# Kernel optimization log

Hardware: AMD Instinct MI355X
Metric: run time of the kernel (lower is better)

The kernel has to match this reference:

```python
import jax, jax.numpy as jnp
import numpy as np
from jax import lax

B, T = 2, 2
BT = B * T
C = 256
NH, DH = 8, 32
NL, NP = 3, 4
NLAYERS = 6
DFF = 1024
SHAPES = [(16, 16), (32, 32), (64, 64)]  # coarse -> fine, last is finest
STARTS = [0, 256, 1280]
LQ = 5376
H4 = W4 = 128
EPS = 1e-5


def setup_inputs():
    key = jax.random.key(0)
    ks = iter(jax.random.split(key, 64))
    def nrm(shape, s=0.02):
        return jax.random.normal(next(ks), shape, jnp.float32) * s
    inp = {}
    for l, (H, W) in enumerate(SHAPES):
        inp[f"src{l}"] = jax.random.normal(next(ks), (BT, C, H, W), jnp.float32)
        inp[f"pos{l}"] = jax.random.normal(next(ks), (BT, C, H, W), jnp.float32)
    inp["mask_features"] = jax.random.normal(next(ks), (B, C, T, H4, W4), jnp.float32)
    inp["level_embed"] = nrm((NL, C), 1.0)
    inp["off_w"] = nrm((NLAYERS, C, NH * NL * NP * 2), 0.01)
    inp["off_b"] = nrm((NLAYERS, NH * NL * NP * 2), 0.1)
    inp["aw_w"] = nrm((NLAYERS, C, NH * NL * NP))
    inp["aw_b"] = jnp.zeros((NLAYERS, NH * NL * NP), jnp.float32)
    inp["val_w"] = nrm((NLAYERS, C, C), 0.05)
    inp["val_b"] = jnp.zeros((NLAYERS, C), jnp.float32)
    inp["out_w"] = nrm((NLAYERS, C, C), 0.05)
    inp["out_b"] = jnp.zeros((NLAYERS, C), jnp.float32)
    inp["ln1_g"] = jnp.ones((NLAYERS, C), jnp.float32)
    inp["ln1_b"] = jnp.zeros((NLAYERS, C), jnp.float32)
    inp["ff1_w"] = nrm((NLAYERS, C, DFF))
    inp["ff1_b"] = jnp.zeros((NLAYERS, DFF), jnp.float32)
    inp["ff2_w"] = nrm((NLAYERS, DFF, C))
    inp["ff2_b"] = jnp.zeros((NLAYERS, C), jnp.float32)
    inp["ln2_g"] = jnp.ones((NLAYERS, C), jnp.float32)
    inp["ln2_b"] = jnp.zeros((NLAYERS, C), jnp.float32)
    inp["lat_w"] = nrm((NLAYERS, C, C, 1, 1), 0.05)
    inp["lat_b"] = jnp.zeros((NLAYERS, C), jnp.float32)
    inp["outc_w"] = nrm((NLAYERS, C, C, 3, 3), 0.02)
    inp["outc_b"] = jnp.zeros((NLAYERS, C), jnp.float32)
    return inp


def _ln(x, g, b):
    m = x.mean(-1, keepdims=True)
    v = ((x - m) ** 2).mean(-1, keepdims=True)
    return (x - m) * lax.rsqrt(v + EPS) * g + b


def _conv(x, w, b, pad):
    y = lax.conv_general_dilated(x, w, (1, 1), [(pad, pad), (pad, pad)],
                                 dimension_numbers=("NCHW", "OIHW", "NCHW"))
    return y + b[None, :, None, None]


def _sample_level(v_l, loc, H, W):
    # v_l: (BT, NH, H*W, DH); loc: (BT, LQ, NH, NP, 2) normalized [0,1]
    # grid_sample bilinear, align_corners=False, zero padding:
    # pixel coord = loc * size - 0.5
    bt, nh, _, dh = v_l.shape
    x = loc[..., 0] * W - 0.5
    y = loc[..., 1] * H - 0.5
    x0 = jnp.floor(x)
    y0 = jnp.floor(y)
    x0i = x0.astype(jnp.int32)
    y0i = y0.astype(jnp.int32)
    fx = (x - x0).transpose(0, 2, 1, 3)[..., None]  # (BT,NH,LQ,NP,1)
    fy = (y - y0).transpose(0, 2, 1, 3)[..., None]
    def gather(ix, iy):
        valid = (ix >= 0) & (ix < W) & (iy >= 0) & (iy < H)
        idx = jnp.clip(iy, 0, H - 1) * W + jnp.clip(ix, 0, W - 1)
        idx = idx.transpose(0, 2, 1, 3)  # (BT,NH,LQ,NP)
        Lq, P = idx.shape[2], idx.shape[3]
        g = jnp.take_along_axis(v_l, idx.reshape(bt, nh, Lq * P)[..., None], axis=2)
        g = g.reshape(bt, nh, Lq, P, dh)
        return g * valid.transpose(0, 2, 1, 3)[..., None]
    v00 = gather(x0i, y0i)
    v01 = gather(x0i + 1, y0i)
    v10 = gather(x0i, y0i + 1)
    v11 = gather(x0i + 1, y0i + 1)
    return (v00 * (1 - fx) * (1 - fy) + v01 * fx * (1 - fy)
            + v10 * (1 - fx) * fy + v11 * fx * fy)


def _ref_points():
    pts = []
    for (H, W) in SHAPES:
        ys = (jnp.arange(H, dtype=jnp.float32) + 0.5) / H
        xs = (jnp.arange(W, dtype=jnp.float32) + 0.5) / W
        gy, gx = jnp.meshgrid(ys, xs, indexing="ij")
        pts.append(jnp.stack([gx.reshape(-1), gy.reshape(-1)], -1))
    return jnp.concatenate(pts, 0)  # (LQ, 2); valid_ratios are all ones


def reference(src0, src1, src2, pos0, pos1, pos2, mask_features, level_embed,
              off_w, off_b, aw_w, aw_b, val_w, val_b, out_w, out_b,
              ln1_g, ln1_b, ff1_w, ff1_b, ff2_w, ff2_b, ln2_g, ln2_b,
              lat_w, lat_b, outc_w, outc_b):
    srcs = [src0, src1, src2]
    poss = [pos0, pos1, pos2]
    output = jnp.concatenate([s.reshape(BT, C, -1).transpose(0, 2, 1) for s in srcs], 1)
    posf = jnp.concatenate(
        [p.reshape(BT, C, -1).transpose(0, 2, 1) + level_embed[l][None, None]
         for l, p in enumerate(poss)], 1)
    refp = _ref_points()
    norm = jnp.array([[W, H] for (H, W) in SHAPES], jnp.float32)  # (NL,2) as (W,H)
    lh, lw = SHAPES[-1]
    for i in range(NLAYERS):
        q = output + posf
        v = (output @ val_w[i] + val_b[i]).reshape(BT, LQ, NH, DH)
        off = (q @ off_w[i] + off_b[i]).reshape(BT, LQ, NH, NL, NP, 2)
        aw = jax.nn.softmax((q @ aw_w[i] + aw_b[i]).reshape(BT, LQ, NH, NL * NP), -1)
        aw = aw.reshape(BT, LQ, NH, NL, NP)
        loc = refp[None, :, None, None, None, :] + off / norm[None, None, None, :, None, :]
        acc = jnp.zeros((BT, NH, LQ, DH), output.dtype)
        for l, (H, W) in enumerate(SHAPES):
            v_l = v[:, STARTS[l]:STARTS[l] + H * W].transpose(0, 2, 1, 3)
            s = _sample_level(v_l, loc[:, :, :, l], H, W)
            acc = acc + (s * aw[:, :, :, l].transpose(0, 2, 1, 3)[..., None]).sum(3)
        attn = acc.transpose(0, 2, 1, 3).reshape(BT, LQ, C) @ out_w[i] + out_b[i]
        output = _ln(output + attn, ln1_g[i], ln1_b[i])
        ff = jax.nn.relu(output @ ff1_w[i] + ff1_b[i]) @ ff2_w[i] + ff2_b[i]
        output = _ln(output + ff, ln2_g[i], ln2_b[i])
        # FPN fusion with the finest transformer level
        lm = output[:, STARTS[-1]:].reshape(BT, lh, lw, C).transpose(0, 3, 1, 2)
        x = mask_features.transpose(0, 2, 1, 3, 4).reshape(B * T, C, H4, W4)
        x = _conv(x, lat_w[i], lat_b[i], 0)
        x = x + jax.image.resize(lm, (BT, C, H4, W4), method="bilinear")
        x = jax.nn.relu(_conv(x, outc_w[i], outc_b[i], 1))
        mask_features = mask_features + x.reshape(B, T, C, H4, W4).transpose(0, 2, 1, 3, 4)
    return output, mask_features
```

## Files before the change

### kernel.cpp

```cpp
#include <hip/hip_runtime.h>

#define DEV __device__ __forceinline__

using f32x4  = __attribute__((ext_vector_type(4))) float;
using bf16x8 = __attribute__((ext_vector_type(8))) short;

static constexpr int kLQ = 5376;

DEV unsigned short f2b(float f) {
  unsigned u = __builtin_bit_cast(unsigned, f);
  u = u + 0x7fffu + ((u >> 16) & 1u);
  return (unsigned short)(u >> 16);
}
DEV float b2f(unsigned short s) {
  unsigned u = ((unsigned)s) << 16;
  return __builtin_bit_cast(float, u);
}

DEV void glds16(const void* g, void* l) {
  __builtin_amdgcn_global_load_lds(
      (const __attribute__((address_space(1))) void*)g,
      (__attribute__((address_space(3))) void*)l, 16, 0, 0);
}

template<int EPI>
__global__ __launch_bounds__(256) void gemm128(
    const unsigned short* __restrict__ A, const unsigned short* __restrict__ Bt,
    const float* __restrict__ bias, void* __restrict__ Cp,
    int M, int N, int K, const float* __restrict__ rsrc)
{
  __shared__ unsigned short As[128 * 32];
  __shared__ unsigned short Bs[128 * 32];
  const int tid = threadIdx.x, lane = tid & 63, wid = tid >> 6;
  const int m0 = blockIdx.x * 128, n0 = blockIdx.y * 128;
  const int wr = wid >> 1, wc = wid & 1;
  const int l15 = lane & 15, lg = lane >> 4;

  const int s0 = wid * 64 + lane, s1 = 256 + s0;
  const int r0 = s0 >> 2, cs0 = (s0 & 3) ^ ((r0 >> 1) & 3);
  const int r1 = s1 >> 2, cs1 = (s1 & 3) ^ ((r1 >> 1) & 3);
  const unsigned short* Ag0 = A + (long)(m0 + r0) * K + cs0 * 8;
  const unsigned short* Ag1 = A + (long)(m0 + r1) * K + cs1 * 8;
  const unsigned short* Bg0 = Bt + (long)(n0 + r0) * K + cs0 * 8;
  const unsigned short* Bg1 = Bt + (long)(n0 + r1) * K + cs1 * 8;
  unsigned short* Al0 = As + (wid * 64) * 8;
  unsigned short* Al1 = As + (256 + wid * 64) * 8;
  unsigned short* Bl0 = Bs + (wid * 64) * 8;
  unsigned short* Bl1 = Bs + (256 + wid * 64) * 8;

  f32x4 acc[4][4];
#pragma unroll
  for (int i = 0; i < 4; i++)
#pragma unroll
    for (int j = 0; j < 4; j++) acc[i][j] = f32x4{0.f, 0.f, 0.f, 0.f};

  for (int k0 = 0; k0 < K; k0 += 32) {
    glds16(Ag0 + k0, Al0);
    glds16(Ag1 + k0, Al1);
    glds16(Bg0 + k0, Bl0);
    glds16(Bg1 + k0, Bl1);
    __syncthreads();
    bf16x8 a[4], b[4];
#pragma unroll
    for (int i = 0; i < 4; i++) {
      int ra = wr * 64 + i * 16 + l15;
      a[i] = *(const bf16x8*)(As + ra * 32 + (lg ^ ((ra >> 1) & 3)) * 8);
      int rb = wc * 64 + i * 16 + l15;
      b[i] = *(const bf16x8*)(Bs + rb * 32 + (lg ^ ((rb >> 1) & 3)) * 8);
    }
#pragma unroll
    for (int mi = 0; mi < 4; mi++)
#pragma unroll
      for (int nj = 0; nj < 4; nj++)
        acc[mi][nj] = __builtin_amdgcn_mfma_f32_16x16x32_bf16(
            a[mi], b[nj], acc[mi][nj], 0, 0, 0);
    __syncthreads();
  }

  int ry0 = 0, ry1 = 0;
  float rfy = 0.f;
  const float* rb0 = nullptr;
  if (EPI == 3) {
    const int bt = m0 >> 14, y = (m0 & 16383) >> 7;
    float sy = y * 0.5f - 0.25f;
    float y0f = floorf(sy);
    rfy = sy - y0f;
    ry0 = min(63, max(0, (int)y0f));
    ry1 = min(63, max(0, (int)y0f + 1));
    rb0 = rsrc + ((long)bt * kLQ + 1280) * 256;
  }

#pragma unroll
  for (int mi = 0; mi < 4; mi++)
#pragma unroll
    for (int nj = 0; nj < 4; nj++) {
      int col = n0 + wc * 64 + nj * 16 + l15;
      if (col >= N) continue;
      float bb = bias[col];
#pragma unroll
      for (int rr = 0; rr < 4; rr++) {
        long row = m0 + wr * 64 + mi * 16 + lg * 4 + rr;
        float v = acc[mi][nj][rr] + bb;
        if (EPI == 2) v = fmaxf(v, 0.f);
        if (EPI == 3) {
          int x = wr * 64 + mi * 16 + lg * 4 + rr;
          float sx = x * 0.5f - 0.25f;
          float x0f = floorf(sx);
          float fx = sx - x0f;
          int x0 = min(63, max(0, (int)x0f)), x1 = min(63, max(0, (int)x0f + 1));
          float v00 = rb0[(long)(ry0 * 64 + x0) * 256 + col];
          float v01 = rb0[(long)(ry0 * 64 + x1) * 256 + col];
          float v10 = rb0[(long)(ry1 * 64 + x0) * 256 + col];
          float v11 = rb0[(long)(ry1 * 64 + x1) * 256 + col];
          v += (1.f - rfy) * ((1.f - fx) * v00 + fx * v01)
             + rfy * ((1.f - fx) * v10 + fx * v11);
        }
        if (EPI == 0) ((float*)Cp)[row * N + col] = v;
        else ((unsigned short*)Cp)[row * N + col] = f2b(v);
      }
    }
}

__global__ __launch_bounds__(256) void conv3x3(
    const unsigned short* __restrict__ xb, const unsigned short* __restrict__ wT,
    const float* __restrict__ bias, float* __restrict__ mf,
    unsigned short* __restrict__ mc)
{
  __shared__ unsigned short As[3 * 128 * 32];
  const int tid = threadIdx.x, lane = tid & 63, wid = tid >> 6;
  const int y = blockIdx.x, c0 = blockIdx.y * 128, bt = blockIdx.z;
  const int wr = wid >> 1, wc = wid & 1;
  const int l15 = lane & 15, lg = lane >> 4;
  const unsigned short* xbb = xb + (long)bt * (16384 * 256);
  const bool zr0 = (y == 0), zr2 = (y == 127);

  f32x4 acc[4][4];
#pragma unroll
  for (int i = 0; i < 4; i++)
#pragma unroll
    for (int j = 0; j < 4; j++) acc[i][j] = f32x4{0.f, 0.f, 0.f, 0.f};

  for (int s = 0; s < 8; s++) {
    const int ci0 = s * 32;
#pragma unroll
    for (int k = 0; k < 6; k++) {
      const int S = k * 256 + tid;
      const int r = S >> 9;
      const int p = (S >> 2) & 127;
      const int cs = (S & 3) ^ ((p >> 1) & 3);
      if ((r == 0 && zr0) || (r == 2 && zr2)) {
        *(uint4*)(As + S * 8) = uint4{0u, 0u, 0u, 0u};
      } else {
        glds16(xbb + ((long)((y + r - 1) * 128 + p) * 256 + ci0 + cs * 8),
               As + (k * 256 + wid * 64) * 8);
      }
    }
    __syncthreads();
#pragma unroll
    for (int r = 0; r < 3; r++) {
#pragma unroll
      for (int dxi = 0; dxi < 3; dxi++) {
        const int t = r * 3 + dxi, dx = dxi - 1;
        const unsigned short* wb = wT + (((long)t * 8 + s) * 256) * 32;
        bf16x8 a[4], b[4];
#pragma unroll
        for (int i = 0; i < 4; i++) {
          const int co_r = c0 + wc * 64 + i * 16 + l15;
          b[i] = *(const bf16x8*)(wb + co_r * 32 + lg * 8);
          const int px = wr * 64 + i * 16 + l15 + dx;
          const int pxc = min(127, max(0, px));
          bf16x8 v = *(const bf16x8*)(
              As + ((r * 128 + pxc) * 4 + (lg ^ ((pxc >> 1) & 3))) * 8);
          if ((unsigned)px >= 128u) v = bf16x8{0, 0, 0, 0, 0, 0, 0, 0};
          a[i] = v;
        }
#pragma unroll
        for (int mi = 0; mi < 4; mi++)
#pragma unroll
          for (int nj = 0; nj < 4; nj++)
            acc[mi][nj] = __builtin_amdgcn_mfma_f32_16x16x32_bf16(
                a[mi], b[nj], acc[mi][nj], 0, 0, 0);
      }
    }
    __syncthreads();
  }

#pragma unroll
  for (int mi = 0; mi < 4; mi++)
#pragma unroll
    for (int nj = 0; nj < 4; nj++) {
      int co = c0 + wc * 64 + nj * 16 + l15;
      float bb = bias[co];
#pragma unroll
      for (int rr = 0; rr < 4; rr++) {
        int x = wr * 64 + mi * 16 + lg * 4 + rr;
        long idx = ((long)bt * 16384 + y * 128 + x) * 256 + co;
        float v = mf[idx] + fmaxf(acc[mi][nj][rr] + bb, 0.f);
        mf[idx] = v;
        mc[idx] = f2b(v);
      }
    }
}

__global__ __launch_bounds__(256) void deform_sample(
    const float* __restrict__ offp, const float* __restrict__ awlog,
    const unsigned short* __restrict__ vp, unsigned short* __restrict__ attn)
{
  const int m = blockIdx.x * 4 + (threadIdx.x >> 6);
  const int t = threadIdx.x & 63;
  const int h = t >> 3, d4 = t & 7;
  const int bt = m / kLQ, q = m % kLQ;
  int pq, Wq;
  if (q < 256)       { pq = q;        Wq = 16; }
  else if (q < 1280) { pq = q - 256;  Wq = 32; }
  else               { pq = q - 1280; Wq = 64; }
  const float refx = ((pq % Wq) + 0.5f) / Wq;
  const float refy = ((pq / Wq) + 0.5f) / Wq;
  const int starts[3] = {0, 256, 1280};
  const int dims[3]   = {16, 32, 64};

  const float4* offr = (const float4*)(offp + (long)m * 192 + h * 24);
  const float4* awr  = (const float4*)(awlog + (long)m * 96 + h * 12);
  float off[24], aw[12];
#pragma unroll
  for (int j = 0; j < 6; j++) {
    float4 v = offr[j];
    off[j * 4] = v.x; off[j * 4 + 1] = v.y; off[j * 4 + 2] = v.z; off[j * 4 + 3] = v.w;
  }
#pragma unroll
  for (int j = 0; j < 3; j++) {
    float4 v = awr[j];
    aw[j * 4] = v.x; aw[j * 4 + 1] = v.y; aw[j * 4 + 2] = v.z; aw[j * 4 + 3] = v.w;
  }
  float mx = aw[0];
#pragma unroll
  for (int j = 1; j < 12; j++) mx = fmaxf(mx, aw[j]);
  float ssum = 0.f;
#pragma unroll
  for (int j = 0; j < 12; j++) { float e = __expf(aw[j] - mx); aw[j] = e; ssum += e; }
  float inv = 1.f / ssum;

  const unsigned short* vb = vp + ((long)bt * kLQ) * 256 + h * 32 + d4 * 4;
  float ax = 0.f, ay = 0.f, az = 0.f, aww = 0.f;
#pragma unroll
  for (int l = 0; l < 3; l++) {
    const int Wl = dims[l];
    const float winv = 1.f / (float)Wl;
    const int st = starts[l];
#pragma unroll
    for (int p = 0; p < 4; p++) {
      float ox = off[l * 8 + p * 2], oy = off[l * 8 + p * 2 + 1];
      float a  = aw[l * 4 + p] * inv;
      float fxp = (refx + ox * winv) * Wl - 0.5f;
      float fyp = (refy + oy * winv) * Wl - 0.5f;
      float x0f = floorf(fxp), y0f = floorf(fyp);
      int x0 = (int)x0f, y0 = (int)y0f;
      float fx = fxp - x0f, fy = fyp - y0f;
      float sx = 0.f, sy = 0.f, sz = 0.f, sw = 0.f;
#pragma unroll
      for (int cy = 0; cy < 2; cy++)
#pragma unroll
        for (int cx = 0; cx < 2; cx++) {
          int ix = x0 + cx, iy = y0 + cy;
          if ((unsigned)ix < (unsigned)Wl && (unsigned)iy < (unsigned)Wl) {
            float w = (cx ? fx : 1.f - fx) * (cy ? fy : 1.f - fy);
            ushort4 u = *(const ushort4*)(vb + (long)(st + iy * Wl + ix) * 256);
            sx += w * b2f(u.x); sy += w * b2f(u.y);
            sz += w * b2f(u.z); sw += w * b2f(u.w);
          }
        }
      ax += a * sx; ay += a * sy; az += a * sz; aww += a * sw;
    }
  }
  ushort4 r;
  r.x = f2b(ax); r.y = f2b(ay); r.z = f2b(az); r.w = f2b(aww);
  *(ushort4*)(attn + (long)m * 256 + h * 32 + d4 * 4) = r;
}

template<bool QB>
__global__ __launch_bounds__(256) void ln_row(
    float* __restrict__ out, const float* __restrict__ delta,
    const float* __restrict__ g, const float* __restrict__ b,
    unsigned short* __restrict__ ob, const float* __restrict__ posf,
    unsigned short* __restrict__ qb)
{
  const long m = blockIdx.x * 4 + (threadIdx.x >> 6);
  const int lane = threadIdx.x & 63;
  const long base = m * 256 + lane * 4;
  float4 a = *(const float4*)(out + base);
  float4 d = *(const float4*)(delta + base);
  float x0 = a.x + d.x, x1 = a.y + d.y, x2 = a.z + d.z, x3 = a.w + d.w;
  float s = x0 + x1 + x2 + x3;
#pragma unroll
  for (int o = 32; o > 0; o >>= 1) s += __shfl_xor(s, o);
  float mean = s * (1.f / 256.f);
  float d0 = x0 - mean, d1 = x1 - mean, d2 = x2 - mean, d3 = x3 - mean;
  float s2 = d0 * d0 + d1 * d1 + d2 * d2 + d3 * d3;
#pragma unroll
  for (int o = 32; o > 0; o >>= 1) s2 += __shfl_xor(s2, o);
  float rs = rsqrtf(s2 * (1.f / 256.f) + 1e-5f);
  float4 gv = *(const float4*)(g + lane * 4);
  float4 bv = *(const float4*)(b + lane * 4);
  float r0 = d0 * rs * gv.x + bv.x, r1 = d1 * rs * gv.y + bv.y;
  float r2 = d2 * rs * gv.z + bv.z, r3 = d3 * rs * gv.w + bv.w;
  *(float4*)(out + base) = float4{r0, r1, r2, r3};
  ushort4 o4; o4.x = f2b(r0); o4.y = f2b(r1); o4.z = f2b(r2); o4.w = f2b(r3);
  *(ushort4*)(ob + base) = o4;
  if (QB) {
    float4 pf = *(const float4*)(posf + base);
    ushort4 q4;
    q4.x = f2b(r0 + pf.x); q4.y = f2b(r1 + pf.y);
    q4.z = f2b(r2 + pf.z); q4.w = f2b(r3 + pf.w);
    *(ushort4*)(qb + base) = q4;
  }
}

__global__ __launch_bounds__(256) void wtrans_pad(
    const float* __restrict__ in, unsigned short* __restrict__ outT,
    int K, int N, int Npad)
{
  int idx = blockIdx.x * 256 + threadIdx.x;
  if (idx >= Npad * K) return;
  int n = idx / K, k = idx % K;
  unsigned short v = 0;
  if (n < N) v = f2b(in[(long)blockIdx.z * K * N + (long)k * N + n]);
  outT[(long)blockIdx.z * Npad * K + idx] = v;
}

__global__ __launch_bounds__(256) void wconvert(
    const float* __restrict__ in, unsigned short* __restrict__ out, int n)
{
  int idx = blockIdx.x * 256 + threadIdx.x;
  if (idx < n) out[idx] = f2b(in[idx]);
}

__global__ __launch_bounds__(256) void wpermconv(
    const float* __restrict__ in, unsigned short* __restrict__ out)
{
  int idx = blockIdx.x * 256 + threadIdx.x;
  const int ci = idx & 255;
  const int co = (idx >> 8) & 255;
  const int t  = (idx >> 16) % 9;
  const int l  = idx / (9 << 16);
  const int s = ci >> 5, cin = ci & 31;
  out[((((long)l * 9 + t) * 8 + s) * 256 + co) * 32 + cin] =
      f2b(in[(((long)l * 256 + co) * 256 + ci) * 9 + t]);
}

__global__ __launch_bounds__(256) void init_level(
    const float* __restrict__ src, const float* __restrict__ pos,
    const float* __restrict__ emb, float* __restrict__ outp,
    float* __restrict__ posf, unsigned short* __restrict__ ob,
    unsigned short* __restrict__ qb, int HW, int start)
{
  __shared__ float t1[32][33];
  __shared__ float t2[32][33];
  const int bt = blockIdx.z;
  const int p0 = blockIdx.x * 32, c0 = blockIdx.y * 32;
  const int tx = threadIdx.x, ty = threadIdx.y;
  const float* sb = src + ((long)bt * 256 + c0) * HW + p0;
  const float* pb = pos + ((long)bt * 256 + c0) * HW + p0;
#pragma unroll
  for (int j = 0; j < 4; j++) {
    int cc = ty + j * 8;
    t1[cc][tx] = sb[(long)cc * HW + tx];
    t2[cc][tx] = pb[(long)cc * HW + tx];
  }
  __syncthreads();
#pragma unroll
  for (int j = 0; j < 4; j++) {
    int pp = ty + j * 8;
    long row = (long)bt * kLQ + start + p0 + pp;
    float v = t1[tx][pp];
    float pv = t2[tx][pp] + emb[c0 + tx];
    outp[row * 256 + c0 + tx] = v;
    ob[row * 256 + c0 + tx] = f2b(v);
    qb[row * 256 + c0 + tx] = f2b(v + pv);
    posf[row * 256 + c0 + tx] = pv;
  }
}

__global__ __launch_bounds__(256) void init_mask(
    const float* __restrict__ in, float* __restrict__ mf,
    unsigned short* __restrict__ mc)
{
  __shared__ float t[32][33];
  const int bt = blockIdx.z, b = bt >> 1, tt = bt & 1;
  const int p0 = blockIdx.x * 32, c0 = blockIdx.y * 32;
  const int tx = threadIdx.x, ty = threadIdx.y;
  const float* base = in + (((long)b * 256 + c0) * 2 + tt) * 16384 + p0;
#pragma unroll
  for (int j = 0; j < 4; j++) {
    int cc = ty + j * 8;
    t[cc][tx] = base[(long)cc * 32768 + tx];
  }
  __syncthreads();
#pragma unroll
  for (int j = 0; j < 4; j++) {
    int pp = ty + j * 8;
    long idx = ((long)bt * 16384 + p0 + pp) * 256 + c0 + tx;
    float v = t[tx][pp];
    mf[idx] = v;
    mc[idx] = f2b(v);
  }
}

__global__ __launch_bounds__(256) void hwc_to_out(
    const float* __restrict__ mf, float* __restrict__ outm)
{
  __shared__ float t[32][33];
  const int bt = blockIdx.z, b = bt >> 1, tt = bt & 1;
  const int p0 = blockIdx.x * 32, c0 = blockIdx.y * 32;
  const int tx = threadIdx.x, ty = threadIdx.y;
#pragma unroll
  for (int j = 0; j < 4; j++) {
    int pp = ty + j * 8;
    t[pp][tx] = mf[((long)bt * 16384 + p0 + pp) * 256 + c0 + tx];
  }
  __syncthreads();
#pragma unroll
  for (int j = 0; j < 4; j++) {
    int cc = ty + j * 8;
    outm[(((long)b * 256 + c0 + cc) * 2 + tt) * 16384 + p0 + tx] = t[tx][cc];
  }
}

extern "C" void kernel_launch(void* const* d_in, const int* in_sizes, int n_in,
                              void* d_out, int out_size, void* d_ws, size_t ws_size,
                              hipStream_t stream)
{
  const float* src[3] = {(const float*)d_in[0], (const float*)d_in[2], (const float*)d_in[4]};
  const float* pos[3] = {(const float*)d_in[1], (const float*)d_in[3], (const float*)d_in[5]};
  const float* mask_in = (const float*)d_in[6];
  const float* lemb    = (const float*)d_in[7];
  const float* off_w   = (const float*)d_in[8];
  const float* off_b   = (const float*)d_in[9];
  const float* aw_w    = (const float*)d_in[10];
  const float* aw_b    = (const float*)d_in[11];
  const float* val_w   = (const float*)d_in[12];
  const float* val_b   = (const float*)d_in[13];
  const float* out_w   = (const float*)d_in[14];
  const float* out_b   = (const float*)d_in[15];
  const float* ln1_g   = (const float*)d_in[16];
  const float* ln1_b   = (const float*)d_in[17];
  const float* ff1_w   = (const float*)d_in[18];
  const float* ff1_b   = (const float*)d_in[19];
  const float* ff2_w   = (const float*)d_in[20];
  const float* ff2_b   = (const float*)d_in[21];
  const float* ln2_g   = (const float*)d_in[22];
  const float* ln2_b   = (const float*)d_in[23];
  const float* lat_w   = (const float*)d_in[24];
  const float* lat_b   = (const float*)d_in[25];
  const float* outc_w  = (const float*)d_in[26];
  const float* outc_b  = (const float*)d_in[27];

  float* outbuf = (float*)d_out;
  float* maskf  = (float*)d_out + 5505024;

  char* wp = (char*)d_ws;
  auto alloc = [&](size_t bytes) {
    char* p = wp;
    wp += (bytes + 255) & ~(size_t)255;
    return p;
  };
  float*          posf  = (float*)alloc(5505024ull * 4);
  unsigned short* qb    = (unsigned short*)alloc(5505024ull * 2);
  unsigned short* ob    = (unsigned short*)alloc(5505024ull * 2);
  unsigned short* vbuf  = (unsigned short*)alloc(5505024ull * 2);
  float*          offb  = (float*)alloc(4128768ull * 4);
  float*          awb   = (float*)alloc(2064384ull * 4);
  unsigned short* attnb = (unsigned short*)alloc(5505024ull * 2);
  float*          tmp1  = (float*)alloc(5505024ull * 4);
  unsigned short* ffh   = (unsigned short*)alloc(22020096ull * 2);
  unsigned short* mc    = (unsigned short*)alloc(16777216ull * 2);
  unsigned short* xb    = (unsigned short*)alloc(16777216ull * 2);
  float*          mfh   = (float*)alloc(16777216ull * 4);
  unsigned short* valT  = (unsigned short*)alloc(6ull * 65536 * 2);
  unsigned short* offT  = (unsigned short*)alloc(6ull * 65536 * 2);
  unsigned short* awT   = (unsigned short*)alloc(6ull * 32768 * 2);
  unsigned short* outT  = (unsigned short*)alloc(6ull * 65536 * 2);
  unsigned short* ff1T  = (unsigned short*)alloc(6ull * 262144 * 2);
  unsigned short* ff2T  = (unsigned short*)alloc(6ull * 262144 * 2);
  unsigned short* latT  = (unsigned short*)alloc(6ull * 65536 * 2);
  unsigned short* outcT = (unsigned short*)alloc(6ull * 589824 * 2);

  wtrans_pad<<<dim3(256, 1, 6), 256, 0, stream>>>(val_w, valT, 256, 256, 256);
  wtrans_pad<<<dim3(256, 1, 6), 256, 0, stream>>>(off_w, offT, 256, 192, 256);
  wtrans_pad<<<dim3(128, 1, 6), 256, 0, stream>>>(aw_w,  awT,  256, 96, 128);
  wtrans_pad<<<dim3(256, 1, 6), 256, 0, stream>>>(out_w, outT, 256, 256, 256);
  wtrans_pad<<<dim3(1024, 1, 6), 256, 0, stream>>>(ff1_w, ff1T, 256, 1024, 1024);
  wtrans_pad<<<dim3(1024, 1, 6), 256, 0, stream>>>(ff2_w, ff2T, 1024, 256, 256);
  wconvert<<<dim3(1536), 256, 0, stream>>>(lat_w, latT, 6 * 65536);
  wpermconv<<<dim3(13824), 256, 0, stream>>>(outc_w, outcT);

  const int hw[3] = {256, 1024, 4096};
  const int st[3] = {0, 256, 1280};
  for (int l = 0; l < 3; l++)
    init_level<<<dim3(hw[l] / 32, 8, 4), dim3(32, 8), 0, stream>>>(
        src[l], pos[l], lemb + l * 256, outbuf, posf, ob, qb, hw[l], st[l]);
  init_mask<<<dim3(512, 8, 4), dim3(32, 8), 0, stream>>>(mask_in, mfh, mc);

  for (int i = 0; i < 6; i++) {
    gemm128<1><<<dim3(168, 2), 256, 0, stream>>>(
        ob, valT + (long)i * 65536, val_b + i * 256, vbuf, 21504, 256, 256, nullptr);
    gemm128<0><<<dim3(168, 2), 256, 0, stream>>>(
        qb, offT + (long)i * 65536, off_b + i * 192, offb, 21504, 192, 256, nullptr);
    gemm128<0><<<dim3(168, 1), 256, 0, stream>>>(
        qb, awT + (long)i * 32768, aw_b + i * 96, awb, 21504, 96, 256, nullptr);
    deform_sample<<<dim3(5376), 256, 0, stream>>>(offb, awb, vbuf, attnb);
    gemm128<0><<<dim3(168, 2), 256, 0, stream>>>(
        attnb, outT + (long)i * 65536, out_b + i * 256, tmp1, 21504, 256, 256, nullptr);
    ln_row<false><<<dim3(5376), 256, 0, stream>>>(
        outbuf, tmp1, ln1_g + i * 256, ln1_b + i * 256, ob, nullptr, nullptr);
    gemm128<2><<<dim3(168, 8), 256, 0, stream>>>(
        ob, ff1T + (long)i * 262144, ff1_b + i * 1024, ffh, 21504, 1024, 256, nullptr);
    gemm128<0><<<dim3(168, 2), 256, 0, stream>>>(
        ffh, ff2T + (long)i * 262144, ff2_b + i * 256, tmp1, 21504, 256, 1024, nullptr);
    ln_row<true><<<dim3(5376), 256, 0, stream>>>(
        outbuf, tmp1, ln2_g + i * 256, ln2_b + i * 256, ob, posf, qb);
    gemm128<3><<<dim3(512, 2), 256, 0, stream>>>(
        mc, latT + (long)i * 65536, lat_b + i * 256, xb, 65536, 256, 256, outbuf);
    conv3x3<<<dim3(128, 2, 4), 256, 0, stream>>>(
        xb, outcT + (long)i * 589824, outc_b + i * 256, mfh, mc);
  }
  hwc_to_out<<<dim3(512, 8, 4), dim3(32, 8), 0, stream>>>(mfh, maskf);
}
```

Baseline: 2.828 ms.

## Drop fp32 mask accumulator and double-buffer conv3x3 LDS staging

The separate fp32 mask_features buffer is removed; the residual is now kept only in the bf16 copy that conv3x3 reads, updates and writes back, and init_mask and hwc_to_out are changed to match. This cuts the fp32 read and write of the full mask tensor on every layer, at the cost of accumulating the residual in bf16 across six layers, which loses precision. Separately, conv3x3 now uses two LDS buffers so the load of the next input-channel slice is issued while MFMAs run on the current one. This doubles the LDS footprint, which may lower occupancy.

```diff
diff --git a/kernel.cpp b/kernel.cpp
--- a/kernel.cpp
+++ b/kernel.cpp
@@ -123,10 +123,9 @@
 
 __global__ __launch_bounds__(256) void conv3x3(
     const unsigned short* __restrict__ xb, const unsigned short* __restrict__ wT,
-    const float* __restrict__ bias, float* __restrict__ mf,
-    unsigned short* __restrict__ mc)
-{
-  __shared__ unsigned short As[3 * 128 * 32];
+    const float* __restrict__ bias, unsigned short* __restrict__ mc)
+{
+  __shared__ unsigned short As[2 * 3 * 128 * 32];
   const int tid = threadIdx.x, lane = tid & 63, wid = tid >> 6;
   const int y = blockIdx.x, c0 = blockIdx.y * 128, bt = blockIdx.z;
   const int wr = wid >> 1, wc = wid & 1;
@@ -140,22 +139,31 @@
 #pragma unroll
     for (int j = 0; j < 4; j++) acc[i][j] = f32x4{0.f, 0.f, 0.f, 0.f};
 
-  for (int s = 0; s < 8; s++) {
+  auto STAGE = [&](int buf, int s) {
     const int ci0 = s * 32;
+    unsigned short* Ab = As + buf * (3 * 128 * 32);
 #pragma unroll
     for (int k = 0; k < 6; k++) {
       const int S = k * 256 + tid;
-      const int r = S >> 9;
+      const int r = k >> 1;
       const int p = (S >> 2) & 127;
       const int cs = (S & 3) ^ ((p >> 1) & 3);
       if ((r == 0 && zr0) || (r == 2 && zr2)) {
-        *(uint4*)(As + S * 8) = uint4{0u, 0u, 0u, 0u};
+        *(uint4*)(Ab + S * 8) = uint4{0u, 0u, 0u, 0u};
       } else {
         glds16(xbb + ((long)((y + r - 1) * 128 + p) * 256 + ci0 + cs * 8),
-               As + (k * 256 + wid * 64) * 8);
+               Ab + (k * 256 + wid * 64) * 8);
       }
     }
-    __syncthreads();
+  };
+
+  STAGE(0, 0);
+  __syncthreads();
+
+  for (int s = 0; s < 8; s++) {
+    const int cur = s & 1;
+    if (s < 7) STAGE(cur ^ 1, s + 1);
+    const unsigned short* Ab = As + cur * (3 * 128 * 32);
 #pragma unroll
     for (int r = 0; r < 3; r++) {
 #pragma unroll
@@ -170,7 +178,7 @@
           const int px = wr * 64 + i * 16 + l15 + dx;
           const int pxc = min(127, max(0, px));
           bf16x8 v = *(const bf16x8*)(
-              As + ((r * 128 + pxc) * 4 + (lg ^ ((pxc >> 1) & 3))) * 8);
+              Ab + ((r * 128 + pxc) * 4 + (lg ^ ((pxc >> 1) & 3))) * 8);
           if ((unsigned)px >= 128u) v = bf16x8{0, 0, 0, 0, 0, 0, 0, 0};
           a[i] = v;
         }
@@ -195,8 +203,7 @@
       for (int rr = 0; rr < 4; rr++) {
         int x = wr * 64 + mi * 16 + lg * 4 + rr;
         long idx = ((long)bt * 16384 + y * 128 + x) * 256 + co;
-        float v = mf[idx] + fmaxf(acc[mi][nj][rr] + bb, 0.f);
-        mf[idx] = v;
+        float v = b2f(mc[idx]) + fmaxf(acc[mi][nj][rr] + bb, 0.f);
         mc[idx] = f2b(v);
       }
     }
@@ -381,8 +388,7 @@
 }
 
 __global__ __launch_bounds__(256) void init_mask(
-    const float* __restrict__ in, float* __restrict__ mf,
-    unsigned short* __restrict__ mc)
+    const float* __restrict__ in, unsigned short* __restrict__ mc)
 {
   __shared__ float t[32][33];
   const int bt = blockIdx.z, b = bt >> 1, tt = bt & 1;
@@ -399,14 +405,12 @@
   for (int j = 0; j < 4; j++) {
     int pp = ty + j * 8;
     long idx = ((long)bt * 16384 + p0 + pp) * 256 + c0 + tx;
-    float v = t[tx][pp];
-    mf[idx] = v;
-    mc[idx] = f2b(v);
+    mc[idx] = f2b(t[tx][pp]);
   }
 }
 
 __global__ __launch_bounds__(256) void hwc_to_out(
-    const float* __restrict__ mf, float* __restrict__ outm)
+    const unsigned short* __restrict__ mc, float* __restrict__ outm)
 {
   __shared__ float t[32][33];
   const int bt = blockIdx.z, b = bt >> 1, tt = bt & 1;
@@ -415,7 +419,7 @@
 #pragma unroll
   for (int j = 0; j < 4; j++) {
     int pp = ty + j * 8;
-    t[pp][tx] = mf[((long)bt * 16384 + p0 + pp) * 256 + c0 + tx];
+    t[pp][tx] = b2f(mc[((long)bt * 16384 + p0 + pp) * 256 + c0 + tx]);
   }
   __syncthreads();
 #pragma unroll
@@ -474,7 +478,6 @@
   unsigned short* ffh   = (unsigned short*)alloc(22020096ull * 2);
   unsigned short* mc    = (unsigned short*)alloc(16777216ull * 2);
   unsigned short* xb    = (unsigned short*)alloc(16777216ull * 2);
-  float*          mfh   = (float*)alloc(16777216ull * 4);
   unsigned short* valT  = (unsigned short*)alloc(6ull * 65536 * 2);
   unsigned short* offT  = (unsigned short*)alloc(6ull * 65536 * 2);
   unsigned short* awT   = (unsigned short*)alloc(6ull * 32768 * 2);
@@ -498,7 +501,7 @@
   for (int l = 0; l < 3; l++)
     init_level<<<dim3(hw[l] / 32, 8, 4), dim3(32, 8), 0, stream>>>(
         src[l], pos[l], lemb + l * 256, outbuf, posf, ob, qb, hw[l], st[l]);
-  init_mask<<<dim3(512, 8, 4), dim3(32, 8), 0, stream>>>(mask_in, mfh, mc);
+  init_mask<<<dim3(512, 8, 4), dim3(32, 8), 0, stream>>>(mask_in, mc);
 
   for (int i = 0; i < 6; i++) {
     gemm128<1><<<dim3(168, 2), 256, 0, stream>>>(
@@ -521,7 +524,7 @@
     gemm128<3><<<dim3(512, 2), 256, 0, stream>>>(
         mc, latT + (long)i * 65536, lat_b + i * 256, xb, 65536, 256, 256, outbuf);
     conv3x3<<<dim3(128, 2, 4), 256, 0, stream>>>(
-        xb, outcT + (long)i * 589824, outc_b + i * 256, mfh, mc);
-  }
-  hwc_to_out<<<dim3(512, 8, 4), dim3(32, 8), 0, stream>>>(mfh, maskf);
-}
+        xb, outcT + (long)i * 589824, outc_b + i * 256, mc);
+  }
+  hwc_to_out<<<dim3(512, 8, 4), dim3(32, 8), 0, stream>>>(mc, maskf);
+}
```

Result: faster. 2.614 ms (-7.6%).
